# Kernel optimization log

Measured on AMD Instinct MI355X. Metric: run time of the kernel, lower is better.

The kernel has to match this reference:

```python
import jax, jax.numpy as jnp
import numpy as np

B, N, D = 16, 4096, 64
LB_TH = 0.01
L2_LAMDA = 0.001
RECONS_LAMDA = 0.2


def _xavier(key, shape):
    fan_in, fan_out = shape[0], shape[1]
    a = float(np.sqrt(6.0 / (fan_in + fan_out)))
    return jax.random.uniform(key, shape, jnp.float32, -a, a)


def setup_inputs() -> dict:
    key = jax.random.key(0)
    k1, k2, k3 = jax.random.split(key, 3)
    X = jax.random.normal(k1, (B, N, D), jnp.float32)
    r_proj = _xavier(k2, (D, D))
    incidence_m = _xavier(k3, (N, N - 1))
    return {"X": X, "r_proj": r_proj, "incidence_m": incidence_m}


def reference(X, r_proj, incidence_m):
    n = incidence_m.shape[0]
    # clamp(min=lb_th) followed by masked_fill(~(v > lb_th), 0) == keep only orig > lb_th
    w = jnp.where(incidence_m > LB_TH, incidence_m, jnp.zeros((), X.dtype))  # [N, N-1]
    # scatter each row's N-1 weights into an NxN matrix, skipping the diagonal
    rows = jnp.arange(n)[:, None]                      # [N,1]
    cols = jnp.arange(n - 1)[None, :]                  # [1,N-1]
    full_cols = cols + (cols >= rows).astype(cols.dtype)  # [N,N-1]
    W = jnp.zeros((n, n), X.dtype).at[rows, full_cols].set(w)
    # per-node projection of master node features: X @ r_proj
    X_proj = jnp.einsum('bnd,de->bne', X, r_proj)      # [B,N,D]
    # neighbor reconstruction for every node at once
    recon = jnp.einsum('ij,bjd->bid', W, X)            # [B,N,D]
    recon_err = jnp.sqrt(jnp.sum((X_proj - recon) ** 2, axis=-1))  # [B,N]
    l1 = jnp.max(jnp.abs(w), axis=1)                   # [N] (max over single-row sum == max abs)
    l2 = jnp.sqrt(jnp.sum(w ** 2, axis=1))             # [N]
    recon_loss = recon_err * RECONS_LAMDA + l1[None, :] + L2_LAMDA * l2[None, :]
    incidence_all = W + jnp.eye(n, dtype=X.dtype)
    return recon_loss, incidence_all
```

## Files before the change

### kernel.cpp

```cpp
#include <hip/hip_runtime.h>
#include <hip/hip_bf16.h>

#define BB 16
#define NN 4096
#define DD 64
#define NM1 4095

typedef __bf16 bf16x8 __attribute__((ext_vector_type(8)));
typedef float f32x4 __attribute__((ext_vector_type(4)));

typedef __attribute__((address_space(1))) const void gas_void;
typedef __attribute__((address_space(3))) void las_void;


__global__ __launch_bounds__(256) void build_kernel(
    const float* __restrict__ inc, float* __restrict__ out_inc,
    __bf16* __restrict__ A16, float* __restrict__ mxa, float* __restrict__ ssa)
{
    int t = threadIdx.x;
    int base = blockIdx.x << 12;
    int rA = (int)((unsigned)base / NM1);
    float pm0 = 0.f, ps0 = 0.f, pm1 = 0.f, ps1 = 0.f;
    #pragma unroll
    for (int j = 0; j < 16; ++j) {
        int f = base + j * 256 + t;
        int i = (int)((unsigned)f / NM1);
        int c = f - i * NM1;
        float x = inc[f];
        float w = x > 0.01f ? x : 0.f;
        int dst = f + i + (c >= i);
        out_inc[dst] = w;
        A16[dst] = (__bf16)w;
        if (i == rA) { pm0 = fmaxf(pm0, w); ps0 += w * w; }
        else         { pm1 = fmaxf(pm1, w); ps1 += w * w; }
    }
    #pragma unroll
    for (int off = 32; off; off >>= 1) {
        pm0 = fmaxf(pm0, __shfl_down(pm0, off));
        ps0 += __shfl_down(ps0, off);
        pm1 = fmaxf(pm1, __shfl_down(pm1, off));
        ps1 += __shfl_down(ps1, off);
    }
    __shared__ float sm0[4], sq0[4], sm1[4], sq1[4];
    int wid = t >> 6;
    if ((t & 63) == 0) { sm0[wid] = pm0; sq0[wid] = ps0; sm1[wid] = pm1; sq1[wid] = ps1; }
    __syncthreads();
    if (t == 0) {
        float m0v = fmaxf(fmaxf(sm0[0], sm0[1]), fmaxf(sm0[2], sm0[3]));
        float s0v = sq0[0] + sq0[1] + sq0[2] + sq0[3];
        float m1v = fmaxf(fmaxf(sm1[0], sm1[1]), fmaxf(sm1[2], sm1[3]));
        float s1v = sq1[0] + sq1[1] + sq1[2] + sq1[3];
        atomicMax((unsigned*)(mxa + rA), __float_as_uint(m0v));
        atomicAdd(ssa + rA, s0v);
        int rB = rA + 1;
        if (rB < NN) {
            atomicMax((unsigned*)(mxa + rB), __float_as_uint(m1v));
            atomicAdd(ssa + rB, s1v);
        }
    }
}

__global__ __launch_bounds__(256) void xt_kernel(
    const float* __restrict__ X, __bf16* __restrict__ XT,
    float* __restrict__ out_inc, __bf16* __restrict__ A16)
{
    __shared__ __bf16 tile[64 * 72];
    int t = threadIdx.x;
    int ntile = blockIdx.x, b = blockIdx.y;
    int n = t >> 2, q = t & 3;
    const float* src = X + ((size_t)b * NN + ntile * 64 + n) * DD + q * 16;
    #pragma unroll
    for (int v = 0; v < 4; ++v) {
        f32x4 u = *(const f32x4*)(src + v * 4);
        #pragma unroll
        for (int j = 0; j < 4; ++j) {
            int d = q * 16 + v * 4 + j;
            tile[d * 72 + n] = (__bf16)u[j];
        }
    }
    __syncthreads();
    int d = t >> 2;
    __bf16* dst = XT + ((size_t)b * DD + d) * NN + ntile * 64 + q * 16;
    *(bf16x8*)dst       = *(bf16x8*)&tile[d * 72 + q * 16];
    *(bf16x8*)(dst + 8) = *(bf16x8*)&tile[d * 72 + q * 16 + 8];
    if (b == 0 && t < 64) {
        int r = ntile * 64 + t;
        out_inc[(size_t)r * NN + r] = 1.0f;
        A16[(size_t)r * NN + r] = (__bf16)1.0f;
    }
}

__global__ __launch_bounds__(256) void gemm_loss_kernel(
    const __bf16* __restrict__ A16, const __bf16* __restrict__ XT,
    const float* __restrict__ X, const float* __restrict__ rproj,
    const float* __restrict__ mxa, const float* __restrict__ ssa,
    float* __restrict__ loss)
{
    __shared__ __bf16 As[64 * 64];
    __shared__ __bf16 Xs[64 * 64];
    __shared__ float sred[64][2];

    int t = threadIdx.x;
    int wave = t >> 6, lane = t & 63;
    int quad = lane >> 4, ln = lane & 15;
    int m0 = blockIdx.x * 64;
    int b  = blockIdx.y;
    int mrow0 = (wave & 1) * 32;
    int ncol0 = (wave >> 1) * 32;
    int sr = lane >> 3;
    int so = lane & 7;

    const __bf16* Abase = A16 + (size_t)m0 * NN;
    const __bf16* Xbase = XT + (size_t)b * DD * NN;

    f32x4 acc[2][2];
    f32x4 zero = {0.f, 0.f, 0.f, 0.f};
    #pragma unroll
    for (int mt = 0; mt < 2; ++mt)
        #pragma unroll
        for (int nt = 0; nt < 2; ++nt) acc[mt][nt] = zero;

    for (int kt = 0; kt < NN / 64; ++kt) {
        int k0 = kt * 64;
        #pragma unroll
        for (int p = 0; p < 2; ++p) {
            int r0 = p * 32 + wave * 8;
            int r  = r0 + sr;
            int og = so ^ (r & 7);
            __builtin_amdgcn_global_load_lds(
                (gas_void*)(Abase + (size_t)r * NN + k0 + og * 8),
                (las_void*)(As + r0 * 64), 16, 0, 0);
            __builtin_amdgcn_global_load_lds(
                (gas_void*)(Xbase + (size_t)r * NN + k0 + og * 8),
                (las_void*)(Xs + r0 * 64), 16, 0, 0);
        }
        __syncthreads();
        #pragma unroll
        for (int kk = 0; kk < 64; kk += 32) {
            int oc = (kk >> 3) + quad;
            bf16x8 af[2], bfr[2];
            #pragma unroll
            for (int mt = 0; mt < 2; ++mt) {
                int r = mrow0 + mt * 16 + ln;
                af[mt] = *(const bf16x8*)&As[r * 64 + ((oc ^ (r & 7)) << 3)];
            }
            #pragma unroll
            for (int nt = 0; nt < 2; ++nt) {
                int n = ncol0 + nt * 16 + ln;
                bfr[nt] = *(const bf16x8*)&Xs[n * 64 + ((oc ^ (n & 7)) << 3)];
            }
            #pragma unroll
            for (int mt = 0; mt < 2; ++mt)
                #pragma unroll
                for (int nt = 0; nt < 2; ++nt)
                    acc[mt][nt] = __builtin_amdgcn_mfma_f32_16x16x32_bf16(
                        af[mt], bfr[nt], acc[mt][nt], 0, 0, 0);
        }
        __syncthreads();
    }

    {
        int rr = t >> 2, q = t & 3;
        const float* xs = X + ((size_t)b * NN + m0 + rr) * DD + q * 16;
        #pragma unroll
        for (int v = 0; v < 2; ++v) {
            f32x4 u0 = *(const f32x4*)(xs + v * 8);
            f32x4 u1 = *(const f32x4*)(xs + v * 8 + 4);
            bf16x8 w;
            #pragma unroll
            for (int j = 0; j < 4; ++j) { w[j] = (__bf16)u0[j]; w[j + 4] = (__bf16)u1[j]; }
            int o = (q * 2 + v) ^ (rr & 7);
            *(bf16x8*)&As[rr * 64 + o * 8] = w;
        }
        const float* rs = rproj + (size_t)rr * DD + q * 16;
        #pragma unroll
        for (int v = 0; v < 4; ++v) {
            f32x4 u = *(const f32x4*)(rs + v * 4);
            #pragma unroll
            for (int j = 0; j < 4; ++j) {
                int d = q * 16 + v * 4 + j;
                float val = u[j] + (d == rr ? 1.0f : 0.0f);
                Xs[d * 64 + (((rr >> 3) ^ (d & 7)) << 3) + (rr & 7)] = (__bf16)val;
            }
        }
    }
    __syncthreads();

    f32x4 xp[2][2];
    #pragma unroll
    for (int mt = 0; mt < 2; ++mt)
        #pragma unroll
        for (int nt = 0; nt < 2; ++nt) xp[mt][nt] = zero;
    #pragma unroll
    for (int kk = 0; kk < DD; kk += 32) {
        int oc = (kk >> 3) + quad;
        bf16x8 af[2], bfr[2];
        #pragma unroll
        for (int mt = 0; mt < 2; ++mt) {
            int r = mrow0 + mt * 16 + ln;
            af[mt] = *(const bf16x8*)&As[r * 64 + ((oc ^ (r & 7)) << 3)];
        }
        #pragma unroll
        for (int nt = 0; nt < 2; ++nt) {
            int n = ncol0 + nt * 16 + ln;
            bfr[nt] = *(const bf16x8*)&Xs[n * 64 + ((oc ^ (n & 7)) << 3)];
        }
        #pragma unroll
        for (int mt = 0; mt < 2; ++mt)
            #pragma unroll
            for (int nt = 0; nt < 2; ++nt)
                xp[mt][nt] = __builtin_amdgcn_mfma_f32_16x16x32_bf16(
                    af[mt], bfr[nt], xp[mt][nt], 0, 0, 0);
    }

    #pragma unroll
    for (int mt = 0; mt < 2; ++mt) {
        #pragma unroll
        for (int rg = 0; rg < 4; ++rg) {
            float s = 0.f;
            #pragma unroll
            for (int nt = 0; nt < 2; ++nt) {
                float df = xp[mt][nt][rg] - acc[mt][nt][rg];
                s += df * df;
            }
            s += __shfl_xor(s, 1);
            s += __shfl_xor(s, 2);
            s += __shfl_xor(s, 4);
            s += __shfl_xor(s, 8);
            if (ln == 0) sred[mrow0 + mt * 16 + quad * 4 + rg][wave >> 1] = s;
        }
    }
    __syncthreads();
    if (t < 64) {
        float s = sred[t][0] + sred[t][1];
        int row = m0 + t;
        loss[(size_t)b * NN + row] =
            0.2f * sqrtf(s) + mxa[row] + 0.001f * sqrtf(ssa[row]);
    }
}

extern "C" void kernel_launch(void* const* d_in, const int* in_sizes, int n_in,
                              void* d_out, int out_size, void* d_ws, size_t ws_size,
                              hipStream_t stream) {
    const float* X   = (const float*)d_in[0];
    const float* r   = (const float*)d_in[1];
    const float* inc = (const float*)d_in[2];
    float* out      = (float*)d_out;
    float* out_loss = out;
    float* out_inc  = out + (size_t)BB * NN;

    char* ws = (char*)d_ws;
    float*  mxa = (float*)ws;
    float*  ssa = (float*)(ws + 16384);
    __bf16* XT  = (__bf16*)(ws + 32768);
    __bf16* A16 = (__bf16*)(ws + 32768 + (size_t)8 * 1024 * 1024);

    hipMemsetAsync(mxa, 0, 32768, stream);

    hipLaunchKernelGGL(build_kernel, dim3(NM1), dim3(256), 0, stream,
                       inc, out_inc, A16, mxa, ssa);
    hipLaunchKernelGGL(xt_kernel, dim3(NN / 64, BB), dim3(256), 0, stream,
                       X, XT, out_inc, A16);
    hipLaunchKernelGGL(gemm_loss_kernel, dim3(NN / 64, BB), dim3(256), 0, stream,
                       A16, XT, X, r, mxa, ssa, out_loss);
}
```

Baseline: 195.2 us.

## Split-K GEMM across waves with per-wave async LDS buffers and fused projection

Each wave now computes the full 64x64 output tile over its own quarter of K, using a private LDS buffer with prefetch issued before the MFMAs and waitcnt-based sync instead of block-wide barriers. Partial accumulators are reduced across waves through LDS, then each wave folds the (I + r_proj) projection in directly with negated weights, loading from global without LDS staging. This removes per-iteration __syncthreads, at the cost of more accumulator registers (launch_bounds 4) and a cross-wave reduction step.

```diff
diff --git a/kernel.cpp b/kernel.cpp
--- a/kernel.cpp
+++ b/kernel.cpp
@@ -90,152 +90,161 @@
     }
 }
 
-__global__ __launch_bounds__(256) void gemm_loss_kernel(
+__global__ __launch_bounds__(256, 4) void gemm_loss_kernel(
     const __bf16* __restrict__ A16, const __bf16* __restrict__ XT,
     const float* __restrict__ X, const float* __restrict__ rproj,
     const float* __restrict__ mxa, const float* __restrict__ ssa,
     float* __restrict__ loss)
 {
-    __shared__ __bf16 As[64 * 64];
-    __shared__ __bf16 Xs[64 * 64];
-    __shared__ float sred[64][2];
+    __shared__ __bf16 lds[4 * 4096];
 
     int t = threadIdx.x;
     int wave = t >> 6, lane = t & 63;
     int quad = lane >> 4, ln = lane & 15;
     int m0 = blockIdx.x * 64;
     int b  = blockIdx.y;
-    int mrow0 = (wave & 1) * 32;
-    int ncol0 = (wave >> 1) * 32;
-    int sr = lane >> 3;
-    int so = lane & 7;
+
+    __bf16* Abuf = lds + wave * 4096;
+    __bf16* Xbuf = Abuf + 2048;
 
     const __bf16* Abase = A16 + (size_t)m0 * NN;
     const __bf16* Xbase = XT + (size_t)b * DD * NN;
 
-    f32x4 acc[2][2];
+    f32x4 acc[4][4];
     f32x4 zero = {0.f, 0.f, 0.f, 0.f};
     #pragma unroll
-    for (int mt = 0; mt < 2; ++mt)
-        #pragma unroll
-        for (int nt = 0; nt < 2; ++nt) acc[mt][nt] = zero;
-
-    for (int kt = 0; kt < NN / 64; ++kt) {
-        int k0 = kt * 64;
-        #pragma unroll
-        for (int p = 0; p < 2; ++p) {
-            int r0 = p * 32 + wave * 8;
-            int r  = r0 + sr;
-            int og = so ^ (r & 7);
+    for (int mt = 0; mt < 4; ++mt)
+        #pragma unroll
+        for (int nt = 0; nt < 4; ++nt) acc[mt][nt] = zero;
+
+    int srow_lo = lane >> 2;
+    int soct = (lane & 3) ^ ((srow_lo >> 1) & 3);
+
+    {
+        int k0 = wave * 32;
+        #pragma unroll
+        for (int p = 0; p < 4; ++p) {
+            int srow = p * 16 + srow_lo;
             __builtin_amdgcn_global_load_lds(
-                (gas_void*)(Abase + (size_t)r * NN + k0 + og * 8),
-                (las_void*)(As + r0 * 64), 16, 0, 0);
+                (gas_void*)(Abase + (size_t)srow * NN + k0 + soct * 8),
+                (las_void*)(Abuf + p * 512), 16, 0, 0);
             __builtin_amdgcn_global_load_lds(
-                (gas_void*)(Xbase + (size_t)r * NN + k0 + og * 8),
-                (las_void*)(Xs + r0 * 64), 16, 0, 0);
-        }
+                (gas_void*)(Xbase + (size_t)srow * NN + k0 + soct * 8),
+                (las_void*)(Xbuf + p * 512), 16, 0, 0);
+        }
+    }
+
+    for (int i = 0; i < 32; ++i) {
+        __builtin_amdgcn_s_waitcnt(0x0F70);
+        bf16x8 af[4], bfr[4];
+        #pragma unroll
+        for (int mt = 0; mt < 4; ++mt) {
+            int r = mt * 16 + ln;
+            int slot = r * 4 + (quad ^ ((ln >> 1) & 3));
+            af[mt] = *(const bf16x8*)&Abuf[slot * 8];
+        }
+        #pragma unroll
+        for (int nt = 0; nt < 4; ++nt) {
+            int n = nt * 16 + ln;
+            int slot = n * 4 + (quad ^ ((ln >> 1) & 3));
+            bfr[nt] = *(const bf16x8*)&Xbuf[slot * 8];
+        }
+        __builtin_amdgcn_s_waitcnt(0xC07F);
+        __builtin_amdgcn_sched_barrier(0);
+        if (i < 31) {
+            int k0 = (wave + 4 * (i + 1)) * 32;
+            #pragma unroll
+            for (int p = 0; p < 4; ++p) {
+                int srow = p * 16 + srow_lo;
+                __builtin_amdgcn_global_load_lds(
+                    (gas_void*)(Abase + (size_t)srow * NN + k0 + soct * 8),
+                    (las_void*)(Abuf + p * 512), 16, 0, 0);
+                __builtin_amdgcn_global_load_lds(
+                    (gas_void*)(Xbase + (size_t)srow * NN + k0 + soct * 8),
+                    (las_void*)(Xbuf + p * 512), 16, 0, 0);
+            }
+        }
+        __builtin_amdgcn_sched_barrier(0);
+        #pragma unroll
+        for (int mt = 0; mt < 4; ++mt)
+            #pragma unroll
+            for (int nt = 0; nt < 4; ++nt)
+                acc[mt][nt] = __builtin_amdgcn_mfma_f32_16x16x32_bf16(
+                    af[mt], bfr[nt], acc[mt][nt], 0, 0, 0);
+    }
+
+    float* red = (float*)lds;
+    #pragma unroll
+    for (int r = 1; r < 4; ++r) {
         __syncthreads();
         #pragma unroll
-        for (int kk = 0; kk < 64; kk += 32) {
-            int oc = (kk >> 3) + quad;
-            bf16x8 af[2], bfr[2];
-            #pragma unroll
-            for (int mt = 0; mt < 2; ++mt) {
-                int r = mrow0 + mt * 16 + ln;
-                af[mt] = *(const bf16x8*)&As[r * 64 + ((oc ^ (r & 7)) << 3)];
-            }
-            #pragma unroll
-            for (int nt = 0; nt < 2; ++nt) {
-                int n = ncol0 + nt * 16 + ln;
-                bfr[nt] = *(const bf16x8*)&Xs[n * 64 + ((oc ^ (n & 7)) << 3)];
-            }
-            #pragma unroll
-            for (int mt = 0; mt < 2; ++mt)
+        for (int p = 0; p < 4; ++p) {
+            if (((p - wave + 4) & 3) == r) {
                 #pragma unroll
-                for (int nt = 0; nt < 2; ++nt)
-                    acc[mt][nt] = __builtin_amdgcn_mfma_f32_16x16x32_bf16(
-                        af[mt], bfr[nt], acc[mt][nt], 0, 0, 0);
+                for (int nt = 0; nt < 4; ++nt)
+                    *(f32x4*)&red[p * 1024 + nt * 256 + lane * 4] = acc[p][nt];
+            }
         }
         __syncthreads();
-    }
-
-    {
-        int rr = t >> 2, q = t & 3;
-        const float* xs = X + ((size_t)b * NN + m0 + rr) * DD + q * 16;
-        #pragma unroll
-        for (int v = 0; v < 2; ++v) {
-            f32x4 u0 = *(const f32x4*)(xs + v * 8);
-            f32x4 u1 = *(const f32x4*)(xs + v * 8 + 4);
-            bf16x8 w;
-            #pragma unroll
-            for (int j = 0; j < 4; ++j) { w[j] = (__bf16)u0[j]; w[j + 4] = (__bf16)u1[j]; }
-            int o = (q * 2 + v) ^ (rr & 7);
-            *(bf16x8*)&As[rr * 64 + o * 8] = w;
-        }
-        const float* rs = rproj + (size_t)rr * DD + q * 16;
-        #pragma unroll
-        for (int v = 0; v < 4; ++v) {
-            f32x4 u = *(const f32x4*)(rs + v * 4);
-            #pragma unroll
-            for (int j = 0; j < 4; ++j) {
-                int d = q * 16 + v * 4 + j;
-                float val = u[j] + (d == rr ? 1.0f : 0.0f);
-                Xs[d * 64 + (((rr >> 3) ^ (d & 7)) << 3) + (rr & 7)] = (__bf16)val;
-            }
-        }
-    }
-    __syncthreads();
-
-    f32x4 xp[2][2];
-    #pragma unroll
-    for (int mt = 0; mt < 2; ++mt)
-        #pragma unroll
-        for (int nt = 0; nt < 2; ++nt) xp[mt][nt] = zero;
+        #pragma unroll
+        for (int p = 0; p < 4; ++p) {
+            if (p == wave) {
+                #pragma unroll
+                for (int nt = 0; nt < 4; ++nt)
+                    acc[p][nt] += *(const f32x4*)&red[p * 1024 + nt * 256 + lane * 4];
+            }
+        }
+    }
+
+    f32x4 dacc[4];
+    #pragma unroll
+    for (int p = 0; p < 4; ++p) {
+        if (p == wave) {
+            #pragma unroll
+            for (int nt = 0; nt < 4; ++nt) dacc[nt] = acc[p][nt];
+        }
+    }
+
     #pragma unroll
     for (int kk = 0; kk < DD; kk += 32) {
-        int oc = (kk >> 3) + quad;
-        bf16x8 af[2], bfr[2];
-        #pragma unroll
-        for (int mt = 0; mt < 2; ++mt) {
-            int r = mrow0 + mt * 16 + ln;
-            af[mt] = *(const bf16x8*)&As[r * 64 + ((oc ^ (r & 7)) << 3)];
-        }
-        #pragma unroll
-        for (int nt = 0; nt < 2; ++nt) {
-            int n = ncol0 + nt * 16 + ln;
-            bfr[nt] = *(const bf16x8*)&Xs[n * 64 + ((oc ^ (n & 7)) << 3)];
-        }
-        #pragma unroll
-        for (int mt = 0; mt < 2; ++mt)
-            #pragma unroll
-            for (int nt = 0; nt < 2; ++nt)
-                xp[mt][nt] = __builtin_amdgcn_mfma_f32_16x16x32_bf16(
-                    af[mt], bfr[nt], xp[mt][nt], 0, 0, 0);
-    }
-
-    #pragma unroll
-    for (int mt = 0; mt < 2; ++mt) {
-        #pragma unroll
-        for (int rg = 0; rg < 4; ++rg) {
-            float s = 0.f;
-            #pragma unroll
-            for (int nt = 0; nt < 2; ++nt) {
-                float df = xp[mt][nt][rg] - acc[mt][nt][rg];
-                s += df * df;
-            }
-            s += __shfl_xor(s, 1);
-            s += __shfl_xor(s, 2);
-            s += __shfl_xor(s, 4);
-            s += __shfl_xor(s, 8);
-            if (ln == 0) sred[mrow0 + mt * 16 + quad * 4 + rg][wave >> 1] = s;
-        }
-    }
-    __syncthreads();
-    if (t < 64) {
-        float s = sred[t][0] + sred[t][1];
-        int row = m0 + t;
-        loss[(size_t)b * NN + row] =
-            0.2f * sqrtf(s) + mxa[row] + 0.001f * sqrtf(ssa[row]);
+        const float* xs = X + ((size_t)b * NN + m0 + wave * 16 + ln) * DD + kk + quad * 8;
+        f32x4 u0 = *(const f32x4*)xs;
+        f32x4 u1 = *(const f32x4*)(xs + 4);
+        bf16x8 afp;
+        #pragma unroll
+        for (int j = 0; j < 4; ++j) { afp[j] = (__bf16)u0[j]; afp[j + 4] = (__bf16)u1[j]; }
+        #pragma unroll
+        for (int nt = 0; nt < 4; ++nt) {
+            bf16x8 bn;
+            #pragma unroll
+            for (int j = 0; j < 8; ++j) {
+                int e = kk + quad * 8 + j;
+                int d = nt * 16 + ln;
+                float val = rproj[(size_t)e * DD + d] + (e == d ? 1.0f : 0.0f);
+                bn[j] = (__bf16)(-val);
+            }
+            dacc[nt] = __builtin_amdgcn_mfma_f32_16x16x32_bf16(
+                afp, bn, dacc[nt], 0, 0, 0);
+        }
+    }
+
+    #pragma unroll
+    for (int rg = 0; rg < 4; ++rg) {
+        float s = 0.f;
+        #pragma unroll
+        for (int nt = 0; nt < 4; ++nt) {
+            float df = dacc[nt][rg];
+            s += df * df;
+        }
+        s += __shfl_xor(s, 1);
+        s += __shfl_xor(s, 2);
+        s += __shfl_xor(s, 4);
+        s += __shfl_xor(s, 8);
+        if (ln == 0) {
+            int row = m0 + wave * 16 + quad * 4 + rg;
+            loss[(size_t)b * NN + row] =
+                0.2f * sqrtf(s) + mxa[row] + 0.001f * sqrtf(ssa[row]);
+        }
     }
 }
 
```

New measurement: 214.3 us. +9.8%, slower.
